# Performance work log

Hardware: AMD Instinct MI355X
Metric: run time of the kernel (lower is better)

## Reference

```python
import jax, jax.numpy as jnp
import numpy as np


def _splat(img, sx, sy, w):
    """One bilinear-gaussian corner splat (scatter-add).
    img: (N,C,H,W); sx,sy,w: (N,1,H,W) integer-valued float shifts + weight.
    Returns (img_warp, one_warp) each (N,C,H,W).
    """
    N, C, H, W = img.shape
    ix = sx.astype(jnp.int32) + jnp.arange(H, dtype=jnp.int32)[None, None, :, None]
    iy = sy.astype(jnp.int32) + jnp.arange(W, dtype=jnp.int32)[None, None, None, :]
    mask = (ix >= 0) & (ix < H) & (iy >= 0) & (iy < W)          # (N,1,H,W)
    ixc = jnp.clip(ix, 0, H - 1)
    iyc = jnp.clip(iy, 0, W - 1)
    nb = jnp.arange(N, dtype=jnp.int32)[:, None, None, None]
    cb = jnp.arange(C, dtype=jnp.int32)[None, :, None, None]
    ids = ((nb * C + cb) * H + ixc) * W + iyc                   # (N,C,H,W)
    ids = jnp.broadcast_to(ids, (N, C, H, W)).reshape(-1)
    wv = jnp.where(mask, w, 0.0)                                # invalid -> 0 contribution
    vals = jnp.broadcast_to(img * wv, (N, C, H, W)).reshape(-1)
    wflat = jnp.broadcast_to(wv, (N, C, H, W)).reshape(-1)
    img_warp = jnp.zeros(N * C * H * W, img.dtype).at[ids].add(vals)
    one_warp = jnp.zeros(N * C * H * W, img.dtype).at[ids].add(wflat)
    return img_warp.reshape(N, C, H, W), one_warp.reshape(N, C, H, W)


def setup_inputs() -> dict:
    key = jax.random.key(0)
    k1, k2 = jax.random.split(key)
    N, C, H, W = 4, 128, 216, 384
    img = jax.random.normal(k1, (N, C, H, W), dtype=jnp.float32)
    # flow displacements of a few pixels magnitude (realistic optical flow)
    flo = jax.random.normal(k2, (N, 2, H, W), dtype=jnp.float32) * 8.0
    return {"img": img, "flo": flo}


def reference(img, flo):
    # y shifts rows (H axis), x shifts cols (W axis), matching the torch code
    y = flo[:, 0:1]    # (N,1,H,W)
    x = flo[:, 1:2]
    x1 = jnp.floor(x); x2 = x1 + 1.0
    y1 = jnp.floor(y); y2 = y1 + 1.0
    w11 = jnp.exp(-((x - x1) ** 2 + (y - y1) ** 2))
    w12 = jnp.exp(-((x - x1) ** 2 + (y - y2) ** 2))
    w21 = jnp.exp(-((x - x2) ** 2 + (y - y1) ** 2))
    w22 = jnp.exp(-((x - x2) ** 2 + (y - y2) ** 2))
    img11, o11 = _splat(img, x1, y1, w11)
    img12, o12 = _splat(img, x1, y2, w12)
    img21, o21 = _splat(img, x2, y1, w21)
    img22, o22 = _splat(img, x2, y2, w22)
    imgw = img11 + img12 + img21 + img22
    o = o11 + o12 + o21 + o22
    return imgw, o
```

## Files before the change

### kernel.cpp

```cpp
#include <hip/hip_runtime.h>


constexpr int N_ = 4, C_ = 128, H_ = 216, W_ = 384;
constexpr int HW    = H_ * W_;
constexpr int TOTAL = N_ * C_ * HW;
constexpr int PIX   = N_ * HW;
constexpr int SCAN_BLOCKS = PIX / 256;

constexpr size_t OFF_IMGT   = 0;
constexpr size_t OFF_OUTT   = (size_t)TOTAL;
constexpr size_t OFF_COUNTS = 2ull * TOTAL;
constexpr size_t OFF_CURSOR = OFF_COUNTS + PIX;
constexpr size_t OFF_OFFS   = OFF_CURSOR + PIX;
constexpr size_t OFF_BS     = OFF_OFFS + PIX;
constexpr size_t OFF_ONES   = OFF_BS + 4096;
constexpr size_t OFF_ES     = OFF_ONES + PIX;
constexpr size_t OFF_EW     = OFF_ES + 4ull * PIX;
constexpr size_t WS_ELEMS   = OFF_EW + 4ull * PIX;
constexpr size_t WS_BYTES   = WS_ELEMS * 4;

__device__ inline void corner_math(float fx, float fy, int& ifx, int& ify,
                                   float& ex0, float& ex1, float& ey0, float& ey1) {
    float fx1 = floorf(fx), fy1 = floorf(fy);
    float dx = fx - fx1, dy = fy - fy1;
    ifx = (int)fx1; ify = (int)fy1;
    ex0 = __expf(-dx * dx);
    ex1 = __expf(-(dx - 1.f) * (dx - 1.f));
    ey0 = __expf(-dy * dy);
    ey1 = __expf(-(dy - 1.f) * (dy - 1.f));
}

__global__ __launch_bounds__(256) void transpose_fwd_k(const float* __restrict__ img,
                                                       float* __restrict__ imgT) {
    __shared__ float tile[32][33];
    int n   = blockIdx.z;
    int hw0 = blockIdx.x * 32;
    int c0  = blockIdx.y * 32;
    const float* src = img  + (size_t)n * C_ * HW;
    float*       dst = imgT + (size_t)n * HW * C_;
    int tx = threadIdx.x, ty = threadIdx.y;
#pragma unroll
    for (int r = 0; r < 32; r += 8)
        tile[ty + r][tx] = src[(size_t)(c0 + ty + r) * HW + hw0 + tx];
    __syncthreads();
#pragma unroll
    for (int r = 0; r < 32; r += 8)
        dst[(size_t)(hw0 + ty + r) * C_ + c0 + tx] = tile[tx][ty + r];
}

__global__ __launch_bounds__(256) void count_k(const float* __restrict__ flo,
                                               unsigned int* __restrict__ counts) {
    int idx = blockIdx.x * 256 + threadIdx.x;
    if (idx >= PIX) return;
    int s = idx % HW, n = idx / HW;
    int h = s / W_, w = s % W_;
    float fy = flo[(n * 2 + 0) * HW + s];
    float fx = flo[(n * 2 + 1) * HW + s];
    int ifx, ify; float ex0, ex1, ey0, ey1;
    corner_math(fx, fy, ifx, ify, ex0, ex1, ey0, ey1);
    int ix = h + ifx, iy = w + ify;
    unsigned int* base = counts + (size_t)n * HW;
    bool bx0 = (unsigned)ix       < (unsigned)H_;
    bool bx1 = (unsigned)(ix + 1) < (unsigned)H_;
    bool by0 = (unsigned)iy       < (unsigned)W_;
    bool by1 = (unsigned)(iy + 1) < (unsigned)W_;
    if (bx0 && by0) atomicAdd(base + ix * W_ + iy, 1u);
    if (bx0 && by1) atomicAdd(base + ix * W_ + iy + 1, 1u);
    if (bx1 && by0) atomicAdd(base + (ix + 1) * W_ + iy, 1u);
    if (bx1 && by1) atomicAdd(base + (ix + 1) * W_ + iy + 1, 1u);
}

__global__ __launch_bounds__(256) void scan_local_k(const unsigned int* __restrict__ counts,
                                                    unsigned int* __restrict__ offs,
                                                    unsigned int* __restrict__ bs) {
    __shared__ unsigned int tmp[256];
    int tid = threadIdx.x;
    int i = blockIdx.x * 256 + tid;
    unsigned int v = counts[i];
    tmp[tid] = v;
    __syncthreads();
    for (int off = 1; off < 256; off <<= 1) {
        unsigned int t = (tid >= off) ? tmp[tid - off] : 0u;
        __syncthreads();
        tmp[tid] += t;
        __syncthreads();
    }
    offs[i] = tmp[tid] - v;
    if (tid == 255) bs[blockIdx.x] = tmp[tid];
}

__global__ __launch_bounds__(256) void scan_bs_k(unsigned int* __restrict__ bs) {
    __shared__ unsigned int tmp[256];
    constexpr int IT = 6;
    int tid = threadIdx.x;
    unsigned int v[IT]; unsigned int sum = 0;
#pragma unroll
    for (int i = 0; i < IT; ++i) {
        int j = tid * IT + i;
        v[i] = (j < SCAN_BLOCKS) ? bs[j] : 0u;
        sum += v[i];
    }
    tmp[tid] = sum;
    __syncthreads();
    for (int off = 1; off < 256; off <<= 1) {
        unsigned int t = (tid >= off) ? tmp[tid - off] : 0u;
        __syncthreads();
        tmp[tid] += t;
        __syncthreads();
    }
    unsigned int run = tmp[tid] - sum;
#pragma unroll
    for (int i = 0; i < IT; ++i) {
        int j = tid * IT + i;
        if (j < SCAN_BLOCKS) { unsigned int old = v[i]; bs[j] = run; run += old; }
    }
}

__global__ __launch_bounds__(256) void scan_add_k(unsigned int* __restrict__ offs,
                                                  const unsigned int* __restrict__ bs) {
    int i = blockIdx.x * 256 + threadIdx.x;
    offs[i] += bs[blockIdx.x];
}

__global__ __launch_bounds__(256) void fill_k(const float* __restrict__ flo,
                                              const unsigned int* __restrict__ offs,
                                              unsigned int* __restrict__ cursor,
                                              unsigned int* __restrict__ entry_s,
                                              float* __restrict__ entry_w) {
    int idx = blockIdx.x * 256 + threadIdx.x;
    if (idx >= PIX) return;
    int s = idx % HW, n = idx / HW;
    int h = s / W_, w = s % W_;
    float fy = flo[(n * 2 + 0) * HW + s];
    float fx = flo[(n * 2 + 1) * HW + s];
    int ifx, ify; float ex0, ex1, ey0, ey1;
    corner_math(fx, fy, ifx, ify, ex0, ex1, ey0, ey1);
    int ix = h + ifx, iy = w + ify;
    bool bx[2] = { (unsigned)ix < (unsigned)H_, (unsigned)(ix + 1) < (unsigned)H_ };
    bool by[2] = { (unsigned)iy < (unsigned)W_, (unsigned)(iy + 1) < (unsigned)W_ };
    float exw[2] = { ex0, ex1 }, eyw[2] = { ey0, ey1 };
#pragma unroll
    for (int a = 0; a < 2; ++a) {
#pragma unroll
        for (int b = 0; b < 2; ++b) {
            if (bx[a] && by[b]) {
                int t = n * HW + (ix + a) * W_ + (iy + b);
                unsigned int slot = atomicAdd(cursor + t, 1u);
                unsigned int e = offs[t] + slot;
                entry_s[e] = (unsigned int)s;
                entry_w[e] = exw[a] * eyw[b];
            }
        }
    }
}

__global__ __launch_bounds__(256) void gather_k(const float* __restrict__ imgT,
                                                const unsigned int* __restrict__ counts,
                                                const unsigned int* __restrict__ offs,
                                                const unsigned int* __restrict__ entry_s,
                                                const float* __restrict__ entry_w,
                                                float* __restrict__ outT,
                                                float* __restrict__ ones_plane) {
    int pl = threadIdx.x >> 5;
    int cg = threadIdx.x & 31;
    int t  = blockIdx.x * 8 + pl;
    int n = t / HW, p = t % HW;
    unsigned int k   = counts[t];
    unsigned int off = offs[t];
    float4 acc = make_float4(0.f, 0.f, 0.f, 0.f);
    float wsum = 0.f;
    const float4* srcBase = (const float4*)(imgT + (size_t)n * HW * C_);
    for (unsigned int j = 0; j < k; ++j) {
        unsigned int s = entry_s[off + j];
        float wgt     = entry_w[off + j];
        float4 v = srcBase[(size_t)s * (C_ / 4) + cg];
        acc.x += wgt * v.x; acc.y += wgt * v.y;
        acc.z += wgt * v.z; acc.w += wgt * v.w;
        wsum += wgt;
    }
    ((float4*)(outT + ((size_t)n * HW + p) * C_))[cg] = acc;
    if (cg == 0) ones_plane[t] = wsum;
}

__global__ __launch_bounds__(256) void transpose_back_k(const float* __restrict__ outT,
                                                        float* __restrict__ out) {
    __shared__ float tile[32][33];
    int n   = blockIdx.z;
    int hw0 = blockIdx.x * 32;
    int c0  = blockIdx.y * 32;
    const float* src = outT + (size_t)n * HW * C_;
    float*       dst = out  + (size_t)n * C_ * HW;
    int tx = threadIdx.x, ty = threadIdx.y;
#pragma unroll
    for (int r = 0; r < 32; r += 8)
        tile[ty + r][tx] = src[(size_t)(hw0 + ty + r) * C_ + c0 + tx];
    __syncthreads();
#pragma unroll
    for (int r = 0; r < 32; r += 8)
        dst[(size_t)(c0 + ty + r) * HW + hw0 + tx] = tile[tx][ty + r];
}

__global__ __launch_bounds__(256) void ones_bcast_k(const float* __restrict__ ones_plane,
                                                    float* __restrict__ out_ones) {
    constexpr int HW4 = HW / 4;
    int idx = blockIdx.x * 256 + threadIdx.x;
    int p  = idx % HW4;
    int cn = idx / HW4;
    int c  = cn % C_;
    int n  = cn / C_;
    const float4* src = (const float4*)(ones_plane + (size_t)n * HW);
    float4*       dst = (float4*)(out_ones + ((size_t)n * C_ + c) * HW);
    dst[p] = src[p];
}

__global__ __launch_bounds__(256) void fb_ones_scatter_k(const float* __restrict__ flo,
                                                         float* __restrict__ out_ones) {
    int idx = blockIdx.x * 256 + threadIdx.x;
    if (idx >= PIX) return;
    int w = idx % W_; int hn = idx / W_; int h = hn % H_; int n = hn / H_;
    float fy = flo[(n * 2 + 0) * HW + h * W_ + w];
    float fx = flo[(n * 2 + 1) * HW + h * W_ + w];
    int ifx, ify; float ex0, ex1, ey0, ey1;
    corner_math(fx, fy, ifx, ify, ex0, ex1, ey0, ey1);
    int ix = h + ifx, iy = w + ify;
    float* plane = out_ones + (size_t)n * C_ * HW;
    if ((unsigned)ix < (unsigned)H_ && (unsigned)iy < (unsigned)W_) atomicAdd(plane + ix * W_ + iy, ex0 * ey0);
    if ((unsigned)ix < (unsigned)H_ && (unsigned)(iy+1) < (unsigned)W_) atomicAdd(plane + ix * W_ + iy + 1, ex0 * ey1);
    if ((unsigned)(ix+1) < (unsigned)H_ && (unsigned)iy < (unsigned)W_) atomicAdd(plane + (ix+1) * W_ + iy, ex1 * ey0);
    if ((unsigned)(ix+1) < (unsigned)H_ && (unsigned)(iy+1) < (unsigned)W_) atomicAdd(plane + (ix+1) * W_ + iy + 1, ex1 * ey1);
}

__global__ __launch_bounds__(256) void fb_img_scatter_k(const float* __restrict__ img,
                                                        const float* __restrict__ flo,
                                                        float* __restrict__ out_img) {
    int idx = blockIdx.x * 256 + threadIdx.x;
    if (idx >= TOTAL) return;
    int w = idx % W_; int rem = idx / W_; int h = rem % H_; rem /= H_;
    int c = rem % C_; int n = rem / C_;
    float fy = flo[(n * 2 + 0) * HW + h * W_ + w];
    float fx = flo[(n * 2 + 1) * HW + h * W_ + w];
    int ifx, ify; float ex0, ex1, ey0, ey1;
    corner_math(fx, fy, ifx, ify, ex0, ex1, ey0, ey1);
    int ix = h + ifx, iy = w + ify;
    float v = img[idx];
    float* plane = out_img + (size_t)(n * C_ + c) * HW;
    if ((unsigned)ix < (unsigned)H_ && (unsigned)iy < (unsigned)W_) atomicAdd(plane + ix * W_ + iy, v * ex0 * ey0);
    if ((unsigned)ix < (unsigned)H_ && (unsigned)(iy+1) < (unsigned)W_) atomicAdd(plane + ix * W_ + iy + 1, v * ex0 * ey1);
    if ((unsigned)(ix+1) < (unsigned)H_ && (unsigned)iy < (unsigned)W_) atomicAdd(plane + (ix+1) * W_ + iy, v * ex1 * ey0);
    if ((unsigned)(ix+1) < (unsigned)H_ && (unsigned)(iy+1) < (unsigned)W_) atomicAdd(plane + (ix+1) * W_ + iy + 1, v * ex1 * ey1);
}

__global__ __launch_bounds__(256) void fb_ones_bcast_k(float* __restrict__ out_ones) {
    constexpr int HW4 = HW / 4;
    constexpr int TOT = N_ * (C_ - 1) * HW4;
    int idx = blockIdx.x * 256 + threadIdx.x;
    if (idx >= TOT) return;
    int p = idx % HW4; int cn = idx / HW4;
    int c = 1 + cn % (C_ - 1); int n = cn / (C_ - 1);
    const float4* src = (const float4*)(out_ones + (size_t)n * C_ * HW);
    float4*       dst = (float4*)(out_ones + ((size_t)n * C_ + c) * HW);
    dst[p] = src[p];
}

extern "C" void kernel_launch(void* const* d_in, const int* in_sizes, int n_in,
                              void* d_out, int out_size, void* d_ws, size_t ws_size,
                              hipStream_t stream) {
    const float* img = (const float*)d_in[0];
    const float* flo = (const float*)d_in[1];
    float* out      = (float*)d_out;
    float* out_img  = out;
    float* out_ones = out + (size_t)TOTAL;

    if (ws_size < WS_BYTES) {
        hipMemsetAsync(out_img, 0, (size_t)TOTAL * sizeof(float), stream);
        for (int n = 0; n < N_; ++n)
            hipMemsetAsync(out_ones + (size_t)n * C_ * HW, 0, HW * sizeof(float), stream);
        fb_ones_scatter_k<<<(PIX + 255) / 256, 256, 0, stream>>>(flo, out_ones);
        fb_img_scatter_k<<<(TOTAL + 255) / 256, 256, 0, stream>>>(img, flo, out_img);
        fb_ones_bcast_k<<<(N_ * (C_ - 1) * (HW / 4) + 255) / 256, 256, 0, stream>>>(out_ones);
        return;
    }

    float* ws = (float*)d_ws;
    float*        imgT    = ws + OFF_IMGT;
    float*        outT    = ws + OFF_OUTT;
    unsigned int* counts  = (unsigned int*)(ws + OFF_COUNTS);
    unsigned int* cursor  = (unsigned int*)(ws + OFF_CURSOR);
    unsigned int* offs    = (unsigned int*)(ws + OFF_OFFS);
    unsigned int* bs      = (unsigned int*)(ws + OFF_BS);
    float*        ones_pl = ws + OFF_ONES;
    unsigned int* entry_s = (unsigned int*)(ws + OFF_ES);
    float*        entry_w = ws + OFF_EW;

    hipMemsetAsync(counts, 0, 2ull * PIX * sizeof(unsigned int), stream);

    dim3 tb(32, 8);
    transpose_fwd_k<<<dim3(HW / 32, C_ / 32, N_), tb, 0, stream>>>(img, imgT);
    count_k<<<SCAN_BLOCKS, 256, 0, stream>>>(flo, counts);
    scan_local_k<<<SCAN_BLOCKS, 256, 0, stream>>>(counts, offs, bs);
    scan_bs_k<<<1, 256, 0, stream>>>(bs);
    scan_add_k<<<SCAN_BLOCKS, 256, 0, stream>>>(offs, bs);
    fill_k<<<SCAN_BLOCKS, 256, 0, stream>>>(flo, offs, cursor, entry_s, entry_w);
    gather_k<<<PIX / 8, 256, 0, stream>>>(imgT, counts, offs, entry_s, entry_w, outT, ones_pl);
    transpose_back_k<<<dim3(HW / 32, C_ / 32, N_), tb, 0, stream>>>(outT, out_img);
    ones_bcast_k<<<(N_ * C_ * (HW / 4) + 255) / 256, 256, 0, stream>>>(ones_pl, out_ones);
}
```

Baseline: 781.9 us.

## Fuse gather with back-transpose and ones broadcast; fold scan add into consumers

The gather kernel now processes 64 pixels per block, stages the per-channel accumulators in a shared-memory tile, and writes both the image output and the broadcast weight-sum output directly in NCHW layout. This removes the intermediate outT buffer, the transpose_back and ones_bcast kernels, and their extra global memory round trips. The separate scan_add kernel is also dropped by adding the block prefix bs[t>>8] at each use in fill and gather. The fallback path is merged into a single scatter kernel that does per-channel atomics to both outputs. In exchange, each gather block walks its 8 pixels per warp serially and uses a large shared tile, which lowers occupancy.

```diff
diff --git a/kernel.cpp b/kernel.cpp
--- a/kernel.cpp
+++ b/kernel.cpp
@@ -8,13 +8,11 @@
 constexpr int SCAN_BLOCKS = PIX / 256;
 
 constexpr size_t OFF_IMGT   = 0;
-constexpr size_t OFF_OUTT   = (size_t)TOTAL;
-constexpr size_t OFF_COUNTS = 2ull * TOTAL;
+constexpr size_t OFF_COUNTS = (size_t)TOTAL;
 constexpr size_t OFF_CURSOR = OFF_COUNTS + PIX;
 constexpr size_t OFF_OFFS   = OFF_CURSOR + PIX;
 constexpr size_t OFF_BS     = OFF_OFFS + PIX;
-constexpr size_t OFF_ONES   = OFF_BS + 4096;
-constexpr size_t OFF_ES     = OFF_ONES + PIX;
+constexpr size_t OFF_ES     = OFF_BS + 4096;
 constexpr size_t OFF_EW     = OFF_ES + 4ull * PIX;
 constexpr size_t WS_ELEMS   = OFF_EW + 4ull * PIX;
 constexpr size_t WS_BYTES   = WS_ELEMS * 4;
@@ -116,14 +114,9 @@
     }
 }
 
-__global__ __launch_bounds__(256) void scan_add_k(unsigned int* __restrict__ offs,
-                                                  const unsigned int* __restrict__ bs) {
-    int i = blockIdx.x * 256 + threadIdx.x;
-    offs[i] += bs[blockIdx.x];
-}
-
 __global__ __launch_bounds__(256) void fill_k(const float* __restrict__ flo,
                                               const unsigned int* __restrict__ offs,
+                                              const unsigned int* __restrict__ bs,
                                               unsigned int* __restrict__ cursor,
                                               unsigned int* __restrict__ entry_s,
                                               float* __restrict__ entry_w) {
@@ -146,7 +139,7 @@
             if (bx[a] && by[b]) {
                 int t = n * HW + (ix + a) * W_ + (iy + b);
                 unsigned int slot = atomicAdd(cursor + t, 1u);
-                unsigned int e = offs[t] + slot;
+                unsigned int e = offs[t] + bs[t >> 8] + slot;
                 entry_s[e] = (unsigned int)s;
                 entry_w[e] = exw[a] * eyw[b];
             }
@@ -154,85 +147,63 @@
     }
 }
 
-__global__ __launch_bounds__(256) void gather_k(const float* __restrict__ imgT,
-                                                const unsigned int* __restrict__ counts,
-                                                const unsigned int* __restrict__ offs,
-                                                const unsigned int* __restrict__ entry_s,
-                                                const float* __restrict__ entry_w,
-                                                float* __restrict__ outT,
-                                                float* __restrict__ ones_plane) {
-    int pl = threadIdx.x >> 5;
-    int cg = threadIdx.x & 31;
-    int t  = blockIdx.x * 8 + pl;
-    int n = t / HW, p = t % HW;
-    unsigned int k   = counts[t];
-    unsigned int off = offs[t];
-    float4 acc = make_float4(0.f, 0.f, 0.f, 0.f);
-    float wsum = 0.f;
+__global__ __launch_bounds__(256) void gather_direct_k(
+        const float* __restrict__ imgT,
+        const unsigned int* __restrict__ counts,
+        const unsigned int* __restrict__ offs,
+        const unsigned int* __restrict__ bs,
+        const unsigned int* __restrict__ entry_s,
+        const float* __restrict__ entry_w,
+        float* __restrict__ out_img,
+        float* __restrict__ out_ones) {
+    __shared__ float tile[64][129];
+    __shared__ float onesb[64];
+    int tid = threadIdx.x;
+    int pl  = tid >> 5;
+    int cg  = tid & 31;
+    int t0  = blockIdx.x * 64;
+    int n   = t0 / HW;
+    int p0  = t0 - n * HW;
     const float4* srcBase = (const float4*)(imgT + (size_t)n * HW * C_);
-    for (unsigned int j = 0; j < k; ++j) {
-        unsigned int s = entry_s[off + j];
-        float wgt     = entry_w[off + j];
-        float4 v = srcBase[(size_t)s * (C_ / 4) + cg];
-        acc.x += wgt * v.x; acc.y += wgt * v.y;
-        acc.z += wgt * v.z; acc.w += wgt * v.w;
-        wsum += wgt;
-    }
-    ((float4*)(outT + ((size_t)n * HW + p) * C_))[cg] = acc;
-    if (cg == 0) ones_plane[t] = wsum;
-}
-
-__global__ __launch_bounds__(256) void transpose_back_k(const float* __restrict__ outT,
-                                                        float* __restrict__ out) {
-    __shared__ float tile[32][33];
-    int n   = blockIdx.z;
-    int hw0 = blockIdx.x * 32;
-    int c0  = blockIdx.y * 32;
-    const float* src = outT + (size_t)n * HW * C_;
-    float*       dst = out  + (size_t)n * C_ * HW;
-    int tx = threadIdx.x, ty = threadIdx.y;
-#pragma unroll
-    for (int r = 0; r < 32; r += 8)
-        tile[ty + r][tx] = src[(size_t)(hw0 + ty + r) * C_ + c0 + tx];
-    __syncthreads();
-#pragma unroll
-    for (int r = 0; r < 32; r += 8)
-        dst[(size_t)(c0 + ty + r) * HW + hw0 + tx] = tile[tx][ty + r];
-}
-
-__global__ __launch_bounds__(256) void ones_bcast_k(const float* __restrict__ ones_plane,
+    for (int j = 0; j < 8; ++j) {
+        int px = j * 8 + pl;
+        int t  = t0 + px;
+        unsigned int k   = counts[t];
+        unsigned int off = offs[t] + bs[t >> 8];
+        float4 acc = make_float4(0.f, 0.f, 0.f, 0.f);
+        float wsum = 0.f;
+        for (unsigned int e = 0; e < k; ++e) {
+            unsigned int s = entry_s[off + e];
+            float wgt     = entry_w[off + e];
+            float4 v = srcBase[(size_t)s * (C_ / 4) + cg];
+            acc.x += wgt * v.x; acc.y += wgt * v.y;
+            acc.z += wgt * v.z; acc.w += wgt * v.w;
+            wsum += wgt;
+        }
+        tile[px][cg * 4 + 0] = acc.x;
+        tile[px][cg * 4 + 1] = acc.y;
+        tile[px][cg * 4 + 2] = acc.z;
+        tile[px][cg * 4 + 3] = acc.w;
+        if (cg == 0) onesb[px] = wsum;
+    }
+    __syncthreads();
+    int i  = tid & 63;
+    int cq = tid >> 6;
+    float onev = onesb[i];
+#pragma unroll
+    for (int cb = 0; cb < 32; ++cb) {
+        int c = cb * 4 + cq;
+        float v = tile[i][c];
+        size_t base = (size_t)(n * C_ + c) * HW + p0 + i;
+        out_img[base]  = v;
+        out_ones[base] = onev;
+    }
+}
+
+__global__ __launch_bounds__(256) void fb_scatter_k(const float* __restrict__ img,
+                                                    const float* __restrict__ flo,
+                                                    float* __restrict__ out_img,
                                                     float* __restrict__ out_ones) {
-    constexpr int HW4 = HW / 4;
-    int idx = blockIdx.x * 256 + threadIdx.x;
-    int p  = idx % HW4;
-    int cn = idx / HW4;
-    int c  = cn % C_;
-    int n  = cn / C_;
-    const float4* src = (const float4*)(ones_plane + (size_t)n * HW);
-    float4*       dst = (float4*)(out_ones + ((size_t)n * C_ + c) * HW);
-    dst[p] = src[p];
-}
-
-__global__ __launch_bounds__(256) void fb_ones_scatter_k(const float* __restrict__ flo,
-                                                         float* __restrict__ out_ones) {
-    int idx = blockIdx.x * 256 + threadIdx.x;
-    if (idx >= PIX) return;
-    int w = idx % W_; int hn = idx / W_; int h = hn % H_; int n = hn / H_;
-    float fy = flo[(n * 2 + 0) * HW + h * W_ + w];
-    float fx = flo[(n * 2 + 1) * HW + h * W_ + w];
-    int ifx, ify; float ex0, ex1, ey0, ey1;
-    corner_math(fx, fy, ifx, ify, ex0, ex1, ey0, ey1);
-    int ix = h + ifx, iy = w + ify;
-    float* plane = out_ones + (size_t)n * C_ * HW;
-    if ((unsigned)ix < (unsigned)H_ && (unsigned)iy < (unsigned)W_) atomicAdd(plane + ix * W_ + iy, ex0 * ey0);
-    if ((unsigned)ix < (unsigned)H_ && (unsigned)(iy+1) < (unsigned)W_) atomicAdd(plane + ix * W_ + iy + 1, ex0 * ey1);
-    if ((unsigned)(ix+1) < (unsigned)H_ && (unsigned)iy < (unsigned)W_) atomicAdd(plane + (ix+1) * W_ + iy, ex1 * ey0);
-    if ((unsigned)(ix+1) < (unsigned)H_ && (unsigned)(iy+1) < (unsigned)W_) atomicAdd(plane + (ix+1) * W_ + iy + 1, ex1 * ey1);
-}
-
-__global__ __launch_bounds__(256) void fb_img_scatter_k(const float* __restrict__ img,
-                                                        const float* __restrict__ flo,
-                                                        float* __restrict__ out_img) {
     int idx = blockIdx.x * 256 + threadIdx.x;
     if (idx >= TOTAL) return;
     int w = idx % W_; int rem = idx / W_; int h = rem % H_; rem /= H_;
@@ -243,23 +214,24 @@
     corner_math(fx, fy, ifx, ify, ex0, ex1, ey0, ey1);
     int ix = h + ifx, iy = w + ify;
     float v = img[idx];
-    float* plane = out_img + (size_t)(n * C_ + c) * HW;
-    if ((unsigned)ix < (unsigned)H_ && (unsigned)iy < (unsigned)W_) atomicAdd(plane + ix * W_ + iy, v * ex0 * ey0);
-    if ((unsigned)ix < (unsigned)H_ && (unsigned)(iy+1) < (unsigned)W_) atomicAdd(plane + ix * W_ + iy + 1, v * ex0 * ey1);
-    if ((unsigned)(ix+1) < (unsigned)H_ && (unsigned)iy < (unsigned)W_) atomicAdd(plane + (ix+1) * W_ + iy, v * ex1 * ey0);
-    if ((unsigned)(ix+1) < (unsigned)H_ && (unsigned)(iy+1) < (unsigned)W_) atomicAdd(plane + (ix+1) * W_ + iy + 1, v * ex1 * ey1);
-}
-
-__global__ __launch_bounds__(256) void fb_ones_bcast_k(float* __restrict__ out_ones) {
-    constexpr int HW4 = HW / 4;
-    constexpr int TOT = N_ * (C_ - 1) * HW4;
-    int idx = blockIdx.x * 256 + threadIdx.x;
-    if (idx >= TOT) return;
-    int p = idx % HW4; int cn = idx / HW4;
-    int c = 1 + cn % (C_ - 1); int n = cn / (C_ - 1);
-    const float4* src = (const float4*)(out_ones + (size_t)n * C_ * HW);
-    float4*       dst = (float4*)(out_ones + ((size_t)n * C_ + c) * HW);
-    dst[p] = src[p];
+    float* pi = out_img  + (size_t)(n * C_ + c) * HW;
+    float* po = out_ones + (size_t)(n * C_ + c) * HW;
+    if ((unsigned)ix < (unsigned)H_ && (unsigned)iy < (unsigned)W_) {
+        atomicAdd(pi + ix * W_ + iy, v * ex0 * ey0);
+        atomicAdd(po + ix * W_ + iy, ex0 * ey0);
+    }
+    if ((unsigned)ix < (unsigned)H_ && (unsigned)(iy + 1) < (unsigned)W_) {
+        atomicAdd(pi + ix * W_ + iy + 1, v * ex0 * ey1);
+        atomicAdd(po + ix * W_ + iy + 1, ex0 * ey1);
+    }
+    if ((unsigned)(ix + 1) < (unsigned)H_ && (unsigned)iy < (unsigned)W_) {
+        atomicAdd(pi + (ix + 1) * W_ + iy, v * ex1 * ey0);
+        atomicAdd(po + (ix + 1) * W_ + iy, ex1 * ey0);
+    }
+    if ((unsigned)(ix + 1) < (unsigned)H_ && (unsigned)(iy + 1) < (unsigned)W_) {
+        atomicAdd(pi + (ix + 1) * W_ + iy + 1, v * ex1 * ey1);
+        atomicAdd(po + (ix + 1) * W_ + iy + 1, ex1 * ey1);
+    }
 }
 
 extern "C" void kernel_launch(void* const* d_in, const int* in_sizes, int n_in,
@@ -272,23 +244,17 @@
     float* out_ones = out + (size_t)TOTAL;
 
     if (ws_size < WS_BYTES) {
-        hipMemsetAsync(out_img, 0, (size_t)TOTAL * sizeof(float), stream);
-        for (int n = 0; n < N_; ++n)
-            hipMemsetAsync(out_ones + (size_t)n * C_ * HW, 0, HW * sizeof(float), stream);
-        fb_ones_scatter_k<<<(PIX + 255) / 256, 256, 0, stream>>>(flo, out_ones);
-        fb_img_scatter_k<<<(TOTAL + 255) / 256, 256, 0, stream>>>(img, flo, out_img);
-        fb_ones_bcast_k<<<(N_ * (C_ - 1) * (HW / 4) + 255) / 256, 256, 0, stream>>>(out_ones);
+        hipMemsetAsync(out, 0, 2ull * TOTAL * sizeof(float), stream);
+        fb_scatter_k<<<(TOTAL + 255) / 256, 256, 0, stream>>>(img, flo, out_img, out_ones);
         return;
     }
 
     float* ws = (float*)d_ws;
     float*        imgT    = ws + OFF_IMGT;
-    float*        outT    = ws + OFF_OUTT;
     unsigned int* counts  = (unsigned int*)(ws + OFF_COUNTS);
     unsigned int* cursor  = (unsigned int*)(ws + OFF_CURSOR);
     unsigned int* offs    = (unsigned int*)(ws + OFF_OFFS);
     unsigned int* bs      = (unsigned int*)(ws + OFF_BS);
-    float*        ones_pl = ws + OFF_ONES;
     unsigned int* entry_s = (unsigned int*)(ws + OFF_ES);
     float*        entry_w = ws + OFF_EW;
 
@@ -299,9 +265,7 @@
     count_k<<<SCAN_BLOCKS, 256, 0, stream>>>(flo, counts);
     scan_local_k<<<SCAN_BLOCKS, 256, 0, stream>>>(counts, offs, bs);
     scan_bs_k<<<1, 256, 0, stream>>>(bs);
-    scan_add_k<<<SCAN_BLOCKS, 256, 0, stream>>>(offs, bs);
-    fill_k<<<SCAN_BLOCKS, 256, 0, stream>>>(flo, offs, cursor, entry_s, entry_w);
-    gather_k<<<PIX / 8, 256, 0, stream>>>(imgT, counts, offs, entry_s, entry_w, outT, ones_pl);
-    transpose_back_k<<<dim3(HW / 32, C_ / 32, N_), tb, 0, stream>>>(outT, out_img);
-    ones_bcast_k<<<(N_ * C_ * (HW / 4) + 255) / 256, 256, 0, stream>>>(ones_pl, out_ones);
-}
+    fill_k<<<SCAN_BLOCKS, 256, 0, stream>>>(flo, offs, bs, cursor, entry_s, entry_w);
+    gather_direct_k<<<PIX / 64, 256, 0, stream>>>(imgT, counts, offs, bs,
+                                                  entry_s, entry_w, out_img, out_ones);
+}
```

Measured after the change: 809.7 us. +3.6%, slower.
